# Optimization experiments

Measured on AMD Instinct MI355X. Metric: run time of the kernel, lower is better.

The kernel has to match this reference:

```python
import jax, jax.numpy as jnp
import numpy as np

N_NODES = 50000
N_EDGES = 1000000
F = 256          # feature_size
NC = 300         # n_content_dims
ED = 64          # embedding_dim = 2**int(log2(F/4))
L = 3            # n_layers


def setup_inputs() -> dict:
    key = jax.random.key(0)
    ks = jax.random.split(key, 20)
    s = 0.05  # weight init scale
    return {
        'node_ids': jnp.arange(N_NODES, dtype=jnp.int32),
        'content': jax.random.normal(ks[0], (N_NODES, NC), jnp.float32),
        'src': jax.random.randint(ks[1], (N_EDGES,), 0, N_NODES, jnp.int32),
        'dst': jax.random.randint(ks[2], (N_EDGES,), 0, N_NODES, jnp.int32),
        'emb': jax.random.normal(ks[3], (N_NODES + 1, ED), jnp.float32) / ED,
        'W_exp': jax.random.normal(ks[4], (F, ED), jnp.float32) * s,
        'b_exp': jnp.zeros((F,), jnp.float32),
        'W_p1': jax.random.normal(ks[5], (NC, NC), jnp.float32) * s,
        'b_p1': jnp.zeros((NC,), jnp.float32),
        'W_p2': jax.random.normal(ks[6], (F, NC), jnp.float32) * s,
        'b_p2': jnp.zeros((F,), jnp.float32),
        'W_conv': jax.random.normal(ks[7], (L, F, 2 * F), jnp.float32) * s,
        'b_conv': jnp.zeros((L, F), jnp.float32),
        'Wo1': jax.random.normal(ks[8], (L - 1, F, F), jnp.float32) * s,
        'bo1': jnp.zeros((L - 1, F), jnp.float32),
        'Wo2': jax.random.normal(ks[9], (L - 1, F, F), jnp.float32) * s,
        'bo2': jnp.zeros((L - 1, F), jnp.float32),
    }


def _lrelu(x):
    return jax.nn.leaky_relu(x, 0.1)


def reference(node_ids, content, src, dst, emb, W_exp, b_exp, W_p1, b_p1,
              W_p2, b_p2, W_conv, b_conv, Wo1, bo1, Wo2, bo2):
    # initial node repr: expansion(node_emb) + proj(content)  (GaussianNoise = identity at eval)
    h = _lrelu(emb[node_ids] @ W_exp.T + b_exp)                 # [N, F]
    c = _lrelu(content @ W_p1.T + b_p1)
    c = _lrelu(c @ W_p2.T + b_p2)
    h = h + c

    ones = jnp.ones((src.shape[0],), h.dtype)
    deg = jax.ops.segment_sum(ones, dst, num_segments=N_NODES)  # in-degree
    w = (deg + 1.0)[:, None]                                    # +1 for self-loop

    for i in range(L):
        # message passing: sum neighbor h (with self-loop), then neighbor mean
        agg = jax.ops.segment_sum(h[src], dst, num_segments=N_NODES) + h  # [N, F]
        h_agg = (agg - h) / jnp.maximum(w - 1.0, 1.0)
        h_concat = jnp.concatenate([h, h_agg], axis=1)          # [N, 2F]
        h_new = h_concat @ W_conv[i].T + b_conv[i]
        if i < L - 1:
            h_new = _lrelu(h_new)
        # L2-normalize rows
        h_new = h_new / jnp.maximum(
            jnp.linalg.norm(h_new, axis=1, keepdims=True), 1e-6)
        if i < L - 1:  # W_out block (non-prediction layers)
            h_new = _lrelu(h_new @ Wo1[i].T + bo1[i])
            h_new = h_new @ Wo2[i].T + bo2[i]
        h = h_new
    return h
```

## Files before the change

kernel.cpp:

```cpp
#include <hip/hip_runtime.h>
#include <stdint.h>

#define NNODES 50000
#define NROWS_PAD 50048
#define NEDGES 1000000
#define FD 256
#define NCPAD 384
#define EDIM 64
#define NSCAN ((NNODES + 255) / 256)

typedef unsigned short u16;
typedef __attribute__((ext_vector_type(8))) short short8;
typedef __attribute__((ext_vector_type(4))) float floatx4;

__device__ __forceinline__ float bf2f(u16 x) {
    union { unsigned u; float f; } c; c.u = ((unsigned)x) << 16; return c.f;
}
__device__ __forceinline__ u16 f2bf(float f) {
    union { float f; unsigned u; } c; c.f = f;
    unsigned u = c.u;
    return (u16)((u + 0x7fffu + ((u >> 16) & 1u)) >> 16);
}
__device__ __forceinline__ void gload16(const u16* g, u16* l) {
    __builtin_amdgcn_global_load_lds(
        (const __attribute__((address_space(1))) void*)g,
        (__attribute__((address_space(3))) void*)l, 16, 0, 0);
}

__global__ void detect_kernel(const u16* p, int* flag) {
    __shared__ int smax;
    if (threadIdx.x == 0) smax = 0;
    __syncthreads();
    int m = 0;
    for (int i = threadIdx.x; i < 8192; i += 256) {
        int e = (p[i] >> 7) & 0xFF;
        m = m > e ? m : e;
    }
    atomicMax(&smax, m);
    __syncthreads();
    if (threadIdx.x == 0) *flag = (smax >= 140) ? 1 : 0;
}

#define NB_CONV 1798
#define NB_CNT4 489
#define PREP_GRID (NB_CONV + NB_CNT4)
__global__ __launch_bounds__(512) void prep_kernel(
    u16* arena, const int* flagp,
    const void* wexp, const void* bexp, const void* wp1, const void* bp1,
    const void* wp2, const void* bp2, const void* wconv, const void* bconv,
    const void* wo1, const void* bo1, const void* wo2, const void* bo2,
    const int* dst, int* deg)
{
    const int bid = blockIdx.x;
    if (bid >= NB_CONV) {
        int base = ((bid - NB_CONV) * 512 + threadIdx.x) * 4;
        if (base < NEDGES) {
            int4 d = *(const int4*)(dst + base);
            atomicAdd(&deg[d.x], 1);
            atomicAdd(&deg[d.y], 1);
            atomicAdd(&deg[d.z], 1);
            atomicAdd(&deg[d.w], 1);
        }
        return;
    }
    const int offs[13]  = {0,16384,16640,164096,164480,262784,263040,
                           656256,657024,788096,788608,919680,920192};
    const int rreal[12] = {256,1,300,1,256,1,768,1,512,1,512,1};
    const int creal[12] = {64,256,300,300,300,256,512,768,256,512,256,512};
    const int cpd[12]   = {64,256,384,384,384,256,512,768,256,512,256,512};
    long gid = (long)bid * 512 + threadIdx.x;
    if (gid >= 920192) return;
    const void* srcs[12] = {wexp,bexp,wp1,bp1,wp2,bp2,wconv,bconv,wo1,bo1,wo2,bo2};
    int fl = *flagp;
    int t = 0;
    #pragma unroll
    for (int i = 1; i < 12; ++i) if (gid >= offs[i]) t = i;
    long local = gid - offs[t];
    int rr = (int)(local / cpd[t]);
    int cc = (int)(local % cpd[t]);
    u16 v = 0;
    if (rr < rreal[t] && cc < creal[t]) {
        long si = (long)rr * creal[t] + cc;
        v = fl ? f2bf(((const float*)srcs[t])[si]) : ((const u16*)srcs[t])[si];
    }
    arena[gid] = v;
}

__global__ __launch_bounds__(256) void scan1_kernel(const int* deg, int* bsum) {
    __shared__ int s[256];
    int t = threadIdx.x;
    int i = blockIdx.x * 256 + t;
    s[t] = (i < NNODES) ? deg[i] : 0;
    __syncthreads();
    #pragma unroll
    for (int off = 128; off > 0; off >>= 1) {
        if (t < off) s[t] += s[t + off];
        __syncthreads();
    }
    if (t == 0) bsum[blockIdx.x] = s[0];
}

__global__ __launch_bounds__(256) void scan2_kernel(int* bsum, int* row_start) {
    __shared__ int s[256];
    int t = threadIdx.x;
    int v = (t < NSCAN) ? bsum[t] : 0;
    s[t] = v;
    __syncthreads();
    for (int off = 1; off < 256; off <<= 1) {
        int x = (t >= off) ? s[t - off] : 0;
        __syncthreads();
        s[t] += x;
        __syncthreads();
    }
    if (t < NSCAN) bsum[t] = s[t] - v;
    if (t == 0) row_start[NNODES] = NEDGES;
}

__global__ __launch_bounds__(256) void scan3_kernel(const int* deg, const int* bsum,
        int* row_start, int* cursor, float* inv_w) {
    __shared__ int s[256];
    int t = threadIdx.x;
    int i = blockIdx.x * 256 + t;
    int v = (i < NNODES) ? deg[i] : 0;
    s[t] = v;
    __syncthreads();
    for (int off = 1; off < 256; off <<= 1) {
        int x = (t >= off) ? s[t - off] : 0;
        __syncthreads();
        s[t] += x;
        __syncthreads();
    }
    if (i < NNODES) {
        int base = bsum[blockIdx.x] + s[t] - v;
        row_start[i] = base;
        cursor[i] = base;
        inv_w[i] = 1.0f / (float)(v > 0 ? v : 1);
    }
}

#define IF_GRID (391 * 7)
__global__ __launch_bounds__(512, 4) void initfill_kernel(
    const void* __restrict__ content, const void* __restrict__ emb,
    const int* __restrict__ flagp,
    const u16* __restrict__ Wp1, const u16* __restrict__ bp1,
    const u16* __restrict__ Wp2, const u16* __restrict__ bp2,
    const u16* __restrict__ Wexp, const u16* __restrict__ bexp,
    u16* __restrict__ hbuf,
    const int* __restrict__ src, const int* __restrict__ dst,
    int* __restrict__ cursor, int* __restrict__ esrc)
{
    __shared__ __align__(16) u16 sA[64 * 64];
    __shared__ __align__(16) u16 sB[384 * 32];
    __shared__ __align__(16) u16 T[64 * 384];

    const int g7 = blockIdx.x / 7, r7 = blockIdx.x % 7;
    if (r7 >= 2) {
        int fb = g7 * 5 + (r7 - 2);
        int e = fb * 512 + threadIdx.x;
        if (e < NEDGES) {
            int v = dst[e];
            int pos = atomicAdd(&cursor[v], 1);
            if ((unsigned)pos < (unsigned)NEDGES) esrc[pos] = src[e];
        }
        return;
    }
    const int bm = (g7 * 2 + r7) * 64;
    const int t = threadIdx.x;
    const int wave = t >> 6, lane = t & 63;
    const int quad = lane >> 4, l16 = lane & 15;
    const int wm = wave >> 2, wn = wave & 3;
    const int lrow = lane >> 2, lcol = (lane & 3) * 8;
    const int fl = *flagp;

    {
        int row = t >> 3;
        int c0 = (t & 7) * 8;
        int gm = bm + row;
        u16 o[8];
        if (gm < NNODES) {
            if (fl) {
                const float* ep = (const float*)emb + (size_t)gm * EDIM + c0;
                float4 x = *(const float4*)ep;
                float4 y = *(const float4*)(ep + 4);
                o[0]=f2bf(x.x); o[1]=f2bf(x.y); o[2]=f2bf(x.z); o[3]=f2bf(x.w);
                o[4]=f2bf(y.x); o[5]=f2bf(y.y); o[6]=f2bf(y.z); o[7]=f2bf(y.w);
            } else {
                const u16* ep = (const u16*)emb + (size_t)gm * EDIM + c0;
                ushort4 x = *(const ushort4*)ep;
                ushort4 y = *(const ushort4*)(ep + 4);
                o[0]=x.x; o[1]=x.y; o[2]=x.z; o[3]=x.w;
                o[4]=y.x; o[5]=y.y; o[6]=y.z; o[7]=y.w;
            }
        } else {
            #pragma unroll
            for (int k = 0; k < 8; ++k) o[k] = 0;
        }
        u16* d = &sA[(row * 64 + c0) ^ ((row & 7) << 3)];
        *(ushort4*)d = (ushort4){o[0], o[1], o[2], o[3]};
        *(ushort4*)(d + 4) = (ushort4){o[4], o[5], o[6], o[7]};
    }
    #pragma unroll
    for (int j = 0; j < 6; ++j) {
        int idx = (j * 512 + t) * 8;
        int row = idx / 384;
        int c0 = idx % 384;
        int gm = bm + row;
        u16 o[8];
        if (gm < NNODES && c0 + 8 <= 300) {
            if (fl) {
                const float* cp = (const float*)content + (size_t)gm * 300 + c0;
                float4 x = *(const float4*)cp;
                float4 y = *(const float4*)(cp + 4);
                o[0]=f2bf(x.x); o[1]=f2bf(x.y); o[2]=f2bf(x.z); o[3]=f2bf(x.w);
                o[4]=f2bf(y.x); o[5]=f2bf(y.y); o[6]=f2bf(y.z); o[7]=f2bf(y.w);
            } else {
                const u16* cp = (const u16*)content + (size_t)gm * 300 + c0;
                ushort4 x = *(const ushort4*)cp;
                ushort4 y = *(const ushort4*)(cp + 4);
                o[0]=x.x; o[1]=x.y; o[2]=x.z; o[3]=x.w;
                o[4]=y.x; o[5]=y.y; o[6]=y.z; o[7]=y.w;
            }
        } else if (gm < NNODES && c0 < 300) {
            #pragma unroll
            for (int k = 0; k < 8; ++k) {
                int c = c0 + k;
                o[k] = (c < 300)
                    ? (fl ? f2bf(((const float*)content)[(size_t)gm * 300 + c])
                          : ((const u16*)content)[(size_t)gm * 300 + c])
                    : (u16)0;
            }
        } else {
            #pragma unroll
            for (int k = 0; k < 8; ++k) o[k] = 0;
        }
        u16* d = &T[(row * 384 + c0) ^ ((row & 7) << 3)];
        *(ushort4*)d = (ushort4){o[0], o[1], o[2], o[3]};
        *(ushort4*)(d + 4) = (ushort4){o[4], o[5], o[6], o[7]};
    }
    __syncthreads();

    floatx4 a1[2][6];
    #pragma unroll
    for (int i = 0; i < 2; ++i)
        #pragma unroll
        for (int j = 0; j < 6; ++j) a1[i][j] = (floatx4){0.f, 0.f, 0.f, 0.f};
    for (int kt = 0; kt < 384; kt += 32) {
        #pragma unroll
        for (int c = 0; c < 3; ++c) {
            int r0 = wave * 48 + c * 16;
            gload16(Wp1 + (size_t)(r0 + lrow) * NCPAD + kt + lcol, &sB[r0 * 32]);
        }
        __syncthreads();
        short8 af[2];
        #pragma unroll
        for (int mt = 0; mt < 2; ++mt) {
            int row = wm * 32 + mt * 16 + l16;
            af[mt] = *(const short8*)&T[(row * 384 + kt + quad * 8) ^ ((row & 7) << 3)];
        }
        #pragma unroll
        for (int nt = 0; nt < 6; ++nt) {
            short8 bf = *(const short8*)&sB[(wn * 96 + nt * 16 + l16) * 32 + quad * 8];
            a1[0][nt] = __builtin_amdgcn_mfma_f32_16x16x32_bf16(af[0], bf, a1[0][nt], 0, 0, 0);
            a1[1][nt] = __builtin_amdgcn_mfma_f32_16x16x32_bf16(af[1], bf, a1[1][nt], 0, 0, 0);
        }
        __syncthreads();
    }
    #pragma unroll
    for (int nt = 0; nt < 6; ++nt) {
        int col = wn * 96 + nt * 16 + l16;
        float bv = bf2f(bp1[col]);
        #pragma unroll
        for (int mt = 0; mt < 2; ++mt)
            #pragma unroll
            for (int rr = 0; rr < 4; ++rr) {
                int row = wm * 32 + mt * 16 + quad * 4 + rr;
                float v = a1[mt][nt][rr] + bv;
                v = v > 0.f ? v : 0.1f * v;
                T[(row * NCPAD + col) ^ ((row & 7) << 3)] = f2bf(v);
            }
    }
    __syncthreads();

    floatx4 a2[2][4];
    #pragma unroll
    for (int i = 0; i < 2; ++i)
        #pragma unroll
        for (int j = 0; j < 4; ++j) a2[i][j] = (floatx4){0.f, 0.f, 0.f, 0.f};
    for (int kt = 0; kt < 384; kt += 32) {
        #pragma unroll
        for (int c = 0; c < 2; ++c) {
            int r0 = wave * 32 + c * 16;
            gload16(Wp2 + (size_t)(r0 + lrow) * NCPAD + kt + lcol, &sB[r0 * 32]);
        }
        __syncthreads();
        short8 af[2];
        #pragma unroll
        for (int mt = 0; mt < 2; ++mt) {
            int row = wm * 32 + mt * 16 + l16;
            af[mt] = *(const short8*)&T[(row * NCPAD + kt + quad * 8) ^ ((row & 7) << 3)];
        }
        #pragma unroll
        for (int nt = 0; nt < 4; ++nt) {
            short8 bf = *(const short8*)&sB[(wn * 64 + nt * 16 + l16) * 32 + quad * 8];
            a2[0][nt] = __builtin_amdgcn_mfma_f32_16x16x32_bf16(af[0], bf, a2[0][nt], 0, 0, 0);
            a2[1][nt] = __builtin_amdgcn_mfma_f32_16x16x32_bf16(af[1], bf, a2[1][nt], 0, 0, 0);
        }
        __syncthreads();
    }

    floatx4 aE[2][4];
    #pragma unroll
    for (int i = 0; i < 2; ++i)
        #pragma unroll
        for (int j = 0; j < 4; ++j) aE[i][j] = (floatx4){0.f, 0.f, 0.f, 0.f};
    for (int kt = 0; kt < 64; kt += 32) {
        #pragma unroll
        for (int c = 0; c < 2; ++c) {
            int r0 = wave * 32 + c * 16;
            gload16(Wexp + (size_t)(r0 + lrow) * EDIM + kt + lcol, &sB[r0 * 32]);
        }
        __syncthreads();
        short8 af[2];
        #pragma unroll
        for (int mt = 0; mt < 2; ++mt) {
            int row = wm * 32 + mt * 16 + l16;
            af[mt] = *(const short8*)&sA[(row * 64 + kt + quad * 8) ^ ((row & 7) << 3)];
        }
        #pragma unroll
        for (int nt = 0; nt < 4; ++nt) {
            short8 bf = *(const short8*)&sB[(wn * 64 + nt * 16 + l16) * 32 + quad * 8];
            aE[0][nt] = __builtin_amdgcn_mfma_f32_16x16x32_bf16(af[0], bf, aE[0][nt], 0, 0, 0);
            aE[1][nt] = __builtin_amdgcn_mfma_f32_16x16x32_bf16(af[1], bf, aE[1][nt], 0, 0, 0);
        }
        __syncthreads();
    }

    #pragma unroll
    for (int nt = 0; nt < 4; ++nt) {
        int col = wn * 64 + nt * 16 + l16;
        float bE = bf2f(bexp[col]), b2 = bf2f(bp2[col]);
        #pragma unroll
        for (int mt = 0; mt < 2; ++mt)
            #pragma unroll
            for (int rr = 0; rr < 4; ++rr) {
                int row = wm * 32 + mt * 16 + quad * 4 + rr;
                int gm = bm + row;
                if (gm < NNODES) {
                    float hE = aE[mt][nt][rr] + bE; hE = hE > 0.f ? hE : 0.1f * hE;
                    float c2 = a2[mt][nt][rr] + b2; c2 = c2 > 0.f ? c2 : 0.1f * c2;
                    hbuf[(size_t)gm * FD + col] = f2bf(hE + c2);
                }
            }
    }
}

__global__ __launch_bounds__(512, 4) void layer_kernel(
    const u16* __restrict__ h, const u16* __restrict__ agg,
    const u16* __restrict__ Wc, const u16* __restrict__ bc,
    const u16* __restrict__ W1, const u16* __restrict__ b1,
    const u16* __restrict__ W2, const u16* __restrict__ b2,
    u16* __restrict__ out)
{
    __shared__ __align__(16) u16 sA[2][64 * 32];
    __shared__ __align__(16) u16 sB[2][256 * 32];
    __shared__ __align__(16) u16 T[64 * 256];
    __shared__ float ssq[4][64];

    const int t = threadIdx.x;
    const int wave = t >> 6, lane = t & 63;
    const int quad = lane >> 4, l16 = lane & 15;
    const int wm = wave >> 2, wn = wave & 3;
    const int lrow = lane >> 2, lcol = (lane & 3) * 8;
    const int bm = blockIdx.x * 64;

    floatx4 acc[2][4];
    #pragma unroll
    for (int i = 0; i < 2; ++i)
        #pragma unroll
        for (int j = 0; j < 4; ++j) acc[i][j] = (floatx4){0.f, 0.f, 0.f, 0.f};

    for (int kt = 0; kt < 512; kt += 64) {
        const u16* Ap = (kt < 256) ? h : agg;
        const int kk = kt & 255;
        {
            int hh = wave & 1, r0 = (wave >> 1) * 16;
            gload16(Ap + (size_t)(bm + r0 + lrow) * 256 + kk + hh * 32 + lcol,
                    &sA[hh][r0 * 32]);
        }
        #pragma unroll
        for (int c = 0; c < 4; ++c) {
            int hh = c >> 1, r0 = wave * 32 + (c & 1) * 16;
            gload16(Wc + (size_t)(r0 + lrow) * 512 + kt + hh * 32 + lcol,
                    &sB[hh][r0 * 32]);
        }
        __syncthreads();
        #pragma unroll
        for (int g = 0; g < 2; ++g) {
            short8 af[2], bf[4];
            #pragma unroll
            for (int mt = 0; mt < 2; ++mt)
                af[mt] = *(const short8*)&sA[g][(wm * 32 + mt * 16 + l16) * 32 + quad * 8];
            #pragma unroll
            for (int nt = 0; nt < 4; ++nt)
                bf[nt] = *(const short8*)&sB[g][(wn * 64 + nt * 16 + l16) * 32 + quad * 8];
            #pragma unroll
            for (int mt = 0; mt < 2; ++mt)
                #pragma unroll
                for (int nt = 0; nt < 4; ++nt)
                    acc[mt][nt] = __builtin_amdgcn_mfma_f32_16x16x32_bf16(af[mt], bf[nt], acc[mt][nt], 0, 0, 0);
        }
        __syncthreads();
    }
    {
        float part[2][4];
        #pragma unroll
        for (int mt = 0; mt < 2; ++mt)
            #pragma unroll
            for (int rr = 0; rr < 4; ++rr) part[mt][rr] = 0.f;
        #pragma unroll
        for (int nt = 0; nt < 4; ++nt) {
            float bv = bf2f(bc[wn * 64 + nt * 16 + l16]);
            #pragma unroll
            for (int mt = 0; mt < 2; ++mt)
                #pragma unroll
                for (int rr = 0; rr < 4; ++rr) {
                    float v = acc[mt][nt][rr] + bv;
                    v = v > 0.f ? v : 0.1f * v;
                    part[mt][rr] += v * v;
                }
        }
        #pragma unroll
        for (int off = 1; off < 16; off <<= 1)
            #pragma unroll
            for (int mt = 0; mt < 2; ++mt)
                #pragma unroll
                for (int rr = 0; rr < 4; ++rr)
                    part[mt][rr] += __shfl_xor(part[mt][rr], off);
        if (l16 == 0)
            #pragma unroll
            for (int mt = 0; mt < 2; ++mt)
                #pragma unroll
                for (int rr = 0; rr < 4; ++rr)
                    ssq[wn][wm * 32 + mt * 16 + quad * 4 + rr] = part[mt][rr];
        __syncthreads();
        #pragma unroll
        for (int mt = 0; mt < 2; ++mt)
            #pragma unroll
            for (int rr = 0; rr < 4; ++rr) {
                int row = wm * 32 + mt * 16 + quad * 4 + rr;
                float s = 1.0f / fmaxf(sqrtf(ssq[0][row] + ssq[1][row] +
                                             ssq[2][row] + ssq[3][row]), 1e-6f);
                #pragma unroll
                for (int nt = 0; nt < 4; ++nt) {
                    int col = wn * 64 + nt * 16 + l16;
                    float v = acc[mt][nt][rr] + bf2f(bc[col]);
                    v = v > 0.f ? v : 0.1f * v;
                    T[(row * 256 + col) ^ ((row & 7) << 3)] = f2bf(v * s);
                }
            }
        __syncthreads();
    }

    #pragma unroll
    for (int i = 0; i < 2; ++i)
        #pragma unroll
        for (int j = 0; j < 4; ++j) acc[i][j] = (floatx4){0.f, 0.f, 0.f, 0.f};
    for (int kt = 0; kt < 256; kt += 64) {
        #pragma unroll
        for (int c = 0; c < 4; ++c) {
            int hh = c >> 1, r0 = wave * 32 + (c & 1) * 16;
            gload16(W1 + (size_t)(r0 + lrow) * 256 + kt + hh * 32 + lcol,
                    &sB[hh][r0 * 32]);
        }
        __syncthreads();
        #pragma unroll
        for (int g = 0; g < 2; ++g) {
            short8 af[2], bf[4];
            #pragma unroll
            for (int mt = 0; mt < 2; ++mt) {
                int row = wm * 32 + mt * 16 + l16;
                af[mt] = *(const short8*)&T[(row * 256 + kt + g * 32 + quad * 8) ^ ((row & 7) << 3)];
            }
            #pragma unroll
            for (int nt = 0; nt < 4; ++nt)
                bf[nt] = *(const short8*)&sB[g][(wn * 64 + nt * 16 + l16) * 32 + quad * 8];
            #pragma unroll
            for (int mt = 0; mt < 2; ++mt)
                #pragma unroll
                for (int nt = 0; nt < 4; ++nt)
                    acc[mt][nt] = __builtin_amdgcn_mfma_f32_16x16x32_bf16(af[mt], bf[nt], acc[mt][nt], 0, 0, 0);
        }
        __syncthreads();
    }
    #pragma unroll
    for (int nt = 0; nt < 4; ++nt) {
        int col = wn * 64 + nt * 16 + l16;
        float bv = bf2f(b1[col]);
        #pragma unroll
        for (int mt = 0; mt < 2; ++mt) {
            #pragma unroll
            for (int r = 0; r < 4; ++r) {
                int row = wm * 32 + mt * 16 + quad * 4 + r;
                float v = acc[mt][nt][r] + bv;
                v = v > 0.f ? v : 0.1f * v;
                T[(row * 256 + col) ^ ((row & 7) << 3)] = f2bf(v);
            }
        }
    }
    __syncthreads();

    #pragma unroll
    for (int i = 0; i < 2; ++i)
        #pragma unroll
        for (int j = 0; j < 4; ++j) acc[i][j] = (floatx4){0.f, 0.f, 0.f, 0.f};
    for (int kt = 0; kt < 256; kt += 64) {
        #pragma unroll
        for (int c = 0; c < 4; ++c) {
            int hh = c >> 1, r0 = wave * 32 + (c & 1) * 16;
            gload16(W2 + (size_t)(r0 + lrow) * 256 + kt + hh * 32 + lcol,
                    &sB[hh][r0 * 32]);
        }
        __syncthreads();
        #pragma unroll
        for (int g = 0; g < 2; ++g) {
            short8 af[2], bf[4];
            #pragma unroll
            for (int mt = 0; mt < 2; ++mt) {
                int row = wm * 32 + mt * 16 + l16;
                af[mt] = *(const short8*)&T[(row * 256 + kt + g * 32 + quad * 8) ^ ((row & 7) << 3)];
            }
            #pragma unroll
            for (int nt = 0; nt < 4; ++nt)
                bf[nt] = *(const short8*)&sB[g][(wn * 64 + nt * 16 + l16) * 32 + quad * 8];
            #pragma unroll
            for (int mt = 0; mt < 2; ++mt)
                #pragma unroll
                for (int nt = 0; nt < 4; ++nt)
                    acc[mt][nt] = __builtin_amdgcn_mfma_f32_16x16x32_bf16(af[mt], bf[nt], acc[mt][nt], 0, 0, 0);
        }
        __syncthreads();
    }
    #pragma unroll
    for (int nt = 0; nt < 4; ++nt) {
        int col = wn * 64 + nt * 16 + l16;
        float bv = bf2f(b2[col]);
        #pragma unroll
        for (int mt = 0; mt < 2; ++mt) {
            #pragma unroll
            for (int r = 0; r < 4; ++r) {
                int row = wm * 32 + mt * 16 + quad * 4 + r;
                int gm = bm + row;
                if (gm < NNODES) {
                    float v = acc[mt][nt][r] + bv;
                    out[(size_t)gm * 256 + col] = f2bf(v);
                }
            }
        }
    }
}

__global__ __launch_bounds__(512, 4) void final_kernel(
    const u16* __restrict__ h, const u16* __restrict__ agg,
    const u16* __restrict__ Wc, const u16* __restrict__ bc,
    float* __restrict__ out)
{
    __shared__ __align__(16) u16 sA[2][64 * 32];
    __shared__ __align__(16) u16 sB[2][256 * 32];
    __shared__ float ssq[4][64];

    const int t = threadIdx.x;
    const int wave = t >> 6, lane = t & 63;
    const int quad = lane >> 4, l16 = lane & 15;
    const int wm = wave >> 2, wn = wave & 3;
    const int lrow = lane >> 2, lcol = (lane & 3) * 8;
    const int bm = blockIdx.x * 64;

    floatx4 acc[2][4];
    #pragma unroll
    for (int i = 0; i < 2; ++i)
        #pragma unroll
        for (int j = 0; j < 4; ++j) acc[i][j] = (floatx4){0.f, 0.f, 0.f, 0.f};

    for (int kt = 0; kt < 512; kt += 64) {
        const u16* Ap = (kt < 256) ? h : agg;
        const int kk = kt & 255;
        {
            int hh = wave & 1, r0 = (wave >> 1) * 16;
            gload16(Ap + (size_t)(bm + r0 + lrow) * 256 + kk + hh * 32 + lcol,
                    &sA[hh][r0 * 32]);
        }
        #pragma unroll
        for (int c = 0; c < 4; ++c) {
            int hh = c >> 1, r0 = wave * 32 + (c & 1) * 16;
            gload16(Wc + (size_t)(r0 + lrow) * 512 + kt + hh * 32 + lcol,
                    &sB[hh][r0 * 32]);
        }
        __syncthreads();
        #pragma unroll
        for (int g = 0; g < 2; ++g) {
            short8 af[2], bf[4];
            #pragma unroll
            for (int mt = 0; mt < 2; ++mt)
                af[mt] = *(const short8*)&sA[g][(wm * 32 + mt * 16 + l16) * 32 + quad * 8];
            #pragma unroll
            for (int nt = 0; nt < 4; ++nt)
                bf[nt] = *(const short8*)&sB[g][(wn * 64 + nt * 16 + l16) * 32 + quad * 8];
            #pragma unroll
            for (int mt = 0; mt < 2; ++mt)
                #pragma unroll
                for (int nt = 0; nt < 4; ++nt)
                    acc[mt][nt] = __builtin_amdgcn_mfma_f32_16x16x32_bf16(af[mt], bf[nt], acc[mt][nt], 0, 0, 0);
        }
        __syncthreads();
    }
    float part[2][4];
    #pragma unroll
    for (int mt = 0; mt < 2; ++mt)
        #pragma unroll
        for (int rr = 0; rr < 4; ++rr) part[mt][rr] = 0.f;
    #pragma unroll
    for (int nt = 0; nt < 4; ++nt) {
        float bv = bf2f(bc[wn * 64 + nt * 16 + l16]);
        #pragma unroll
        for (int mt = 0; mt < 2; ++mt)
            #pragma unroll
            for (int rr = 0; rr < 4; ++rr) {
                float v = acc[mt][nt][rr] + bv;
                part[mt][rr] += v * v;
            }
    }
    #pragma unroll
    for (int off = 1; off < 16; off <<= 1)
        #pragma unroll
        for (int mt = 0; mt < 2; ++mt)
            #pragma unroll
            for (int rr = 0; rr < 4; ++rr)
                part[mt][rr] += __shfl_xor(part[mt][rr], off);
    if (l16 == 0)
        #pragma unroll
        for (int mt = 0; mt < 2; ++mt)
            #pragma unroll
            for (int rr = 0; rr < 4; ++rr)
                ssq[wn][wm * 32 + mt * 16 + quad * 4 + rr] = part[mt][rr];
    __syncthreads();
    #pragma unroll
    for (int mt = 0; mt < 2; ++mt)
        #pragma unroll
        for (int rr = 0; rr < 4; ++rr) {
            int row = wm * 32 + mt * 16 + quad * 4 + rr;
            int gm = bm + row;
            float s = 1.0f / fmaxf(sqrtf(ssq[0][row] + ssq[1][row] +
                                         ssq[2][row] + ssq[3][row]), 1e-6f);
            if (gm < NNODES) {
                #pragma unroll
                for (int nt = 0; nt < 4; ++nt) {
                    int col = wn * 64 + nt * 16 + l16;
                    out[(size_t)gm * 256 + col] = (acc[mt][nt][rr] + bf2f(bc[col])) * s;
                }
            }
        }
}

__global__ __launch_bounds__(256) void agg_kernel(
    const u16* h, const int* row_start, const int* esrc,
    const float* inv_w, u16* out)
{
    int gid = blockIdx.x * blockDim.x + threadIdx.x;
    int wid = __builtin_amdgcn_readfirstlane(gid >> 6);
    int lane = threadIdx.x & 63;
    if (wid >= NNODES) return;
    int e0 = row_start[wid], e1 = row_start[wid + 1];
    e0 = max(0, min(e0, NEDGES));
    e1 = max(e0, min(e1, NEDGES));
    float a0 = 0.f, a1 = 0.f, a2 = 0.f, a3 = 0.f;
    int e = e0;
    for (; e + 8 <= e1; e += 8) {
        int u[8];
        #pragma unroll
        for (int k = 0; k < 8; ++k) {
            u[k] = esrc[e + k];
            if ((unsigned)u[k] >= (unsigned)NNODES) u[k] = 0;
        }
        ushort4 tv[8];
        #pragma unroll
        for (int k = 0; k < 8; ++k)
            tv[k] = *(const ushort4*)(h + (size_t)u[k] * FD + lane * 4);
        #pragma unroll
        for (int k = 0; k < 8; ++k) {
            a0 += bf2f(tv[k].x); a1 += bf2f(tv[k].y);
            a2 += bf2f(tv[k].z); a3 += bf2f(tv[k].w);
        }
    }
    for (; e + 2 <= e1; e += 2) {
        int u0 = esrc[e + 0]; if ((unsigned)u0 >= (unsigned)NNODES) u0 = 0;
        int u1 = esrc[e + 1]; if ((unsigned)u1 >= (unsigned)NNODES) u1 = 0;
        ushort4 t0 = *(const ushort4*)(h + (size_t)u0 * FD + lane * 4);
        ushort4 t1 = *(const ushort4*)(h + (size_t)u1 * FD + lane * 4);
        a0 += bf2f(t0.x) + bf2f(t1.x);
        a1 += bf2f(t0.y) + bf2f(t1.y);
        a2 += bf2f(t0.z) + bf2f(t1.z);
        a3 += bf2f(t0.w) + bf2f(t1.w);
    }
    for (; e < e1; ++e) {
        int u = esrc[e];
        if ((unsigned)u >= (unsigned)NNODES) u = 0;
        ushort4 tv = *(const ushort4*)(h + (size_t)u * FD + lane * 4);
        a0 += bf2f(tv.x); a1 += bf2f(tv.y); a2 += bf2f(tv.z); a3 += bf2f(tv.w);
    }
    float s = inv_w[wid];
    ushort4 ov;
    ov.x = f2bf(a0 * s); ov.y = f2bf(a1 * s); ov.z = f2bf(a2 * s); ov.w = f2bf(a3 * s);
    *(ushort4*)(out + (size_t)wid * FD + lane * 4) = ov;
}

extern "C" void kernel_launch(void* const* d_in, const int* in_sizes, int n_in,
                              void* d_out, int out_size, void* d_ws, size_t ws_size,
                              hipStream_t stream) {
    const void* content = d_in[1];
    const int* src      = (const int*)d_in[2];
    const int* dst      = (const int*)d_in[3];
    const void* emb     = d_in[4];

    char* ws = (char*)d_ws;
    u16* arena = (u16*)(ws);
    u16* hbuf  = (u16*)(ws + 1840640);
    u16* buf2  = (u16*)(ws + 27465216);
    int*   deg    = (int*)(ws + 78714368);
    int*   rs     = (int*)(ws + 78914560);
    int*   cursor = (int*)(ws + 79114752);
    float* inv_w  = (float*)(ws + 79314944);
    int*   esrc   = (int*)(ws + 79515136);
    int*   bsum   = (int*)(ws + 83515648);
    int*   flag   = (int*)(ws + 83516672);

    u16* aWexp  = arena;            u16* aBexp  = arena + 16384;
    u16* aWp1   = arena + 16640;    u16* aBp1   = arena + 164096;
    u16* aWp2   = arena + 164480;   u16* aBp2   = arena + 262784;
    u16* aWconv = arena + 263040;   u16* aBconv = arena + 656256;
    u16* aWo1   = arena + 657024;   u16* aBo1   = arena + 788096;
    u16* aWo2   = arena + 788608;   u16* aBo2   = arena + 919680;

    const int MB64 = NROWS_PAD / 64;

    detect_kernel<<<1, 256, 0, stream>>>((const u16*)content, flag);
    hipMemsetAsync(deg, 0, (size_t)NNODES * 4, stream);
    prep_kernel<<<PREP_GRID, 512, 0, stream>>>(arena, flag,
        d_in[5], d_in[6], d_in[7], d_in[8], d_in[9], d_in[10], d_in[11],
        d_in[12], d_in[13], d_in[14], d_in[15], d_in[16], dst, deg);

    scan1_kernel<<<NSCAN, 256, 0, stream>>>(deg, bsum);
    scan2_kernel<<<1, 256, 0, stream>>>(bsum, rs);
    scan3_kernel<<<NSCAN, 256, 0, stream>>>(deg, bsum, rs, cursor, inv_w);

    initfill_kernel<<<IF_GRID, 512, 0, stream>>>(content, emb, flag,
        aWp1, aBp1, aWp2, aBp2, aWexp, aBexp, hbuf, src, dst, cursor, esrc);

    for (int i = 0; i < 3; ++i) {
        agg_kernel<<<(NNODES * 64) / 256, 256, 0, stream>>>(hbuf, rs, esrc, inv_w, buf2);
        if (i < 2) {
            layer_kernel<<<dim3(MB64), dim3(512), 0, stream>>>(
                hbuf, buf2,
                aWconv + (size_t)i * FD * 2 * FD, aBconv + (size_t)i * FD,
                aWo1 + (size_t)i * FD * FD, aBo1 + (size_t)i * FD,
                aWo2 + (size_t)i * FD * FD, aBo2 + (size_t)i * FD,
                hbuf);
        } else {
            final_kernel<<<dim3(MB64), dim3(512), 0, stream>>>(
                hbuf, buf2,
                aWconv + (size_t)i * FD * 2 * FD, aBconv + (size_t)i * FD,
                (float*)d_out);
        }
    }
}
```

Measured before the change: 651.3 us.

## Shrink GEMM K-tile to raise occupancy and fuse prologue launches

The layer and final GEMM kernels now stage a single 32-wide K slice instead of two, which halves the shared-memory tiles and raises the launch-bounds occupancy hint from 4 to 6 blocks. The degree memset is folded into the detect kernel, and the two scan kernels after the block-sum pass are merged so each block reduces its own prefix of block sums. These cuts are meant to remove launch overhead and let more blocks overlap memory latency. In exchange there are twice as many barriers per K loop and less work between each sync.

```diff
diff --git a/kernel.cpp b/kernel.cpp
--- a/kernel.cpp
+++ b/kernel.cpp
@@ -27,13 +27,16 @@
         (__attribute__((address_space(3))) void*)l, 16, 0, 0);
 }
 
-__global__ void detect_kernel(const u16* p, int* flag) {
+__global__ __launch_bounds__(256) void detect_kernel(const u16* p, int* flag, int* deg) {
+    int i = blockIdx.x * 256 + threadIdx.x;
+    if (i < NNODES) deg[i] = 0;
+    if (blockIdx.x != 0) return;
     __shared__ int smax;
     if (threadIdx.x == 0) smax = 0;
     __syncthreads();
     int m = 0;
-    for (int i = threadIdx.x; i < 8192; i += 256) {
-        int e = (p[i] >> 7) & 0xFF;
+    for (int k = threadIdx.x; k < 8192; k += 256) {
+        int e = (p[k] >> 7) & 0xFF;
         m = m > e ? m : e;
     }
     atomicMax(&smax, m);
@@ -100,11 +103,25 @@
     if (t == 0) bsum[blockIdx.x] = s[0];
 }
 
-__global__ __launch_bounds__(256) void scan2_kernel(int* bsum, int* row_start) {
+__global__ __launch_bounds__(256) void scan23_kernel(const int* deg, const int* bsum,
+        int* row_start, int* cursor, float* inv_w) {
     __shared__ int s[256];
+    __shared__ int sbase;
     int t = threadIdx.x;
-    int v = (t < NSCAN) ? bsum[t] : 0;
+    int b = blockIdx.x;
+    int v = (t < b && t < NSCAN) ? bsum[t] : 0;
     s[t] = v;
+    __syncthreads();
+    #pragma unroll
+    for (int off = 128; off > 0; off >>= 1) {
+        if (t < off) s[t] += s[t + off];
+        __syncthreads();
+    }
+    if (t == 0) sbase = s[0];
+    __syncthreads();
+    int i = b * 256 + t;
+    int d = (i < NNODES) ? deg[i] : 0;
+    s[t] = d;
     __syncthreads();
     for (int off = 1; off < 256; off <<= 1) {
         int x = (t >= off) ? s[t - off] : 0;
@@ -112,30 +129,13 @@
         s[t] += x;
         __syncthreads();
     }
-    if (t < NSCAN) bsum[t] = s[t] - v;
-    if (t == 0) row_start[NNODES] = NEDGES;
-}
-
-__global__ __launch_bounds__(256) void scan3_kernel(const int* deg, const int* bsum,
-        int* row_start, int* cursor, float* inv_w) {
-    __shared__ int s[256];
-    int t = threadIdx.x;
-    int i = blockIdx.x * 256 + t;
-    int v = (i < NNODES) ? deg[i] : 0;
-    s[t] = v;
-    __syncthreads();
-    for (int off = 1; off < 256; off <<= 1) {
-        int x = (t >= off) ? s[t - off] : 0;
-        __syncthreads();
-        s[t] += x;
-        __syncthreads();
-    }
     if (i < NNODES) {
-        int base = bsum[blockIdx.x] + s[t] - v;
+        int base = sbase + s[t] - d;
         row_start[i] = base;
         cursor[i] = base;
-        inv_w[i] = 1.0f / (float)(v > 0 ? v : 1);
-    }
+        inv_w[i] = 1.0f / (float)(d > 0 ? d : 1);
+    }
+    if (b == 0 && t == 0) row_start[NNODES] = NEDGES;
 }
 
 #define IF_GRID (391 * 7)
@@ -354,15 +354,15 @@
     }
 }
 
-__global__ __launch_bounds__(512, 4) void layer_kernel(
+__global__ __launch_bounds__(512, 6) void layer_kernel(
     const u16* __restrict__ h, const u16* __restrict__ agg,
     const u16* __restrict__ Wc, const u16* __restrict__ bc,
     const u16* __restrict__ W1, const u16* __restrict__ b1,
     const u16* __restrict__ W2, const u16* __restrict__ b2,
     u16* __restrict__ out)
 {
-    __shared__ __align__(16) u16 sA[2][64 * 32];
-    __shared__ __align__(16) u16 sB[2][256 * 32];
+    __shared__ __align__(16) u16 sA[64 * 32];
+    __shared__ __align__(16) u16 sB[256 * 32];
     __shared__ __align__(16) u16 T[64 * 256];
     __shared__ float ssq[4][64];
 
@@ -379,36 +379,30 @@
         #pragma unroll
         for (int j = 0; j < 4; ++j) acc[i][j] = (floatx4){0.f, 0.f, 0.f, 0.f};
 
-    for (int kt = 0; kt < 512; kt += 64) {
+    for (int kt = 0; kt < 512; kt += 32) {
         const u16* Ap = (kt < 256) ? h : agg;
         const int kk = kt & 255;
-        {
-            int hh = wave & 1, r0 = (wave >> 1) * 16;
-            gload16(Ap + (size_t)(bm + r0 + lrow) * 256 + kk + hh * 32 + lcol,
-                    &sA[hh][r0 * 32]);
-        }
-        #pragma unroll
-        for (int c = 0; c < 4; ++c) {
-            int hh = c >> 1, r0 = wave * 32 + (c & 1) * 16;
-            gload16(Wc + (size_t)(r0 + lrow) * 512 + kt + hh * 32 + lcol,
-                    &sB[hh][r0 * 32]);
-        }
-        __syncthreads();
-        #pragma unroll
-        for (int g = 0; g < 2; ++g) {
-            short8 af[2], bf[4];
-            #pragma unroll
-            for (int mt = 0; mt < 2; ++mt)
-                af[mt] = *(const short8*)&sA[g][(wm * 32 + mt * 16 + l16) * 32 + quad * 8];
+        if (wave < 4)
+            gload16(Ap + (size_t)(bm + wave * 16 + lrow) * 256 + kk + lcol,
+                    &sA[(wave * 16) * 32]);
+        #pragma unroll
+        for (int c = 0; c < 2; ++c) {
+            int r0 = wave * 32 + c * 16;
+            gload16(Wc + (size_t)(r0 + lrow) * 512 + kt + lcol, &sB[r0 * 32]);
+        }
+        __syncthreads();
+        short8 af[2], bf[4];
+        #pragma unroll
+        for (int mt = 0; mt < 2; ++mt)
+            af[mt] = *(const short8*)&sA[(wm * 32 + mt * 16 + l16) * 32 + quad * 8];
+        #pragma unroll
+        for (int nt = 0; nt < 4; ++nt)
+            bf[nt] = *(const short8*)&sB[(wn * 64 + nt * 16 + l16) * 32 + quad * 8];
+        #pragma unroll
+        for (int mt = 0; mt < 2; ++mt)
             #pragma unroll
             for (int nt = 0; nt < 4; ++nt)
-                bf[nt] = *(const short8*)&sB[g][(wn * 64 + nt * 16 + l16) * 32 + quad * 8];
-            #pragma unroll
-            for (int mt = 0; mt < 2; ++mt)
-                #pragma unroll
-                for (int nt = 0; nt < 4; ++nt)
-                    acc[mt][nt] = __builtin_amdgcn_mfma_f32_16x16x32_bf16(af[mt], bf[nt], acc[mt][nt], 0, 0, 0);
-        }
+                acc[mt][nt] = __builtin_amdgcn_mfma_f32_16x16x32_bf16(af[mt], bf[nt], acc[mt][nt], 0, 0, 0);
         __syncthreads();
     }
     {
@@ -465,31 +459,27 @@
     for (int i = 0; i < 2; ++i)
         #pragma unroll
         for (int j = 0; j < 4; ++j) acc[i][j] = (floatx4){0.f, 0.f, 0.f, 0.f};
-    for (int kt = 0; kt < 256; kt += 64) {
-        #pragma unroll
-        for (int c = 0; c < 4; ++c) {
-            int hh = c >> 1, r0 = wave * 32 + (c & 1) * 16;
-            gload16(W1 + (size_t)(r0 + lrow) * 256 + kt + hh * 32 + lcol,
-                    &sB[hh][r0 * 32]);
-        }
-        __syncthreads();
-        #pragma unroll
-        for (int g = 0; g < 2; ++g) {
-            short8 af[2], bf[4];
-            #pragma unroll
-            for (int mt = 0; mt < 2; ++mt) {
-                int row = wm * 32 + mt * 16 + l16;
-                af[mt] = *(const short8*)&T[(row * 256 + kt + g * 32 + quad * 8) ^ ((row & 7) << 3)];
-            }
+    for (int kt = 0; kt < 256; kt += 32) {
+        #pragma unroll
+        for (int c = 0; c < 2; ++c) {
+            int r0 = wave * 32 + c * 16;
+            gload16(W1 + (size_t)(r0 + lrow) * 256 + kt + lcol, &sB[r0 * 32]);
+        }
+        __syncthreads();
+        short8 af[2], bf[4];
+        #pragma unroll
+        for (int mt = 0; mt < 2; ++mt) {
+            int row = wm * 32 + mt * 16 + l16;
+            af[mt] = *(const short8*)&T[(row * 256 + kt + quad * 8) ^ ((row & 7) << 3)];
+        }
+        #pragma unroll
+        for (int nt = 0; nt < 4; ++nt)
+            bf[nt] = *(const short8*)&sB[(wn * 64 + nt * 16 + l16) * 32 + quad * 8];
+        #pragma unroll
+        for (int mt = 0; mt < 2; ++mt)
             #pragma unroll
             for (int nt = 0; nt < 4; ++nt)
-                bf[nt] = *(const short8*)&sB[g][(wn * 64 + nt * 16 + l16) * 32 + quad * 8];
-            #pragma unroll
-            for (int mt = 0; mt < 2; ++mt)
-                #pragma unroll
-                for (int nt = 0; nt < 4; ++nt)
-                    acc[mt][nt] = __builtin_amdgcn_mfma_f32_16x16x32_bf16(af[mt], bf[nt], acc[mt][nt], 0, 0, 0);
-        }
+                acc[mt][nt] = __builtin_amdgcn_mfma_f32_16x16x32_bf16(af[mt], bf[nt], acc[mt][nt], 0, 0, 0);
         __syncthreads();
     }
     #pragma unroll
@@ -513,31 +503,27 @@
     for (int i = 0; i < 2; ++i)
         #pragma unroll
         for (int j = 0; j < 4; ++j) acc[i][j] = (floatx4){0.f, 0.f, 0.f, 0.f};
-    for (int kt = 0; kt < 256; kt += 64) {
-        #pragma unroll
-        for (int c = 0; c < 4; ++c) {
-            int hh = c >> 1, r0 = wave * 32 + (c & 1) * 16;
-            gload16(W2 + (size_t)(r0 + lrow) * 256 + kt + hh * 32 + lcol,
-                    &sB[hh][r0 * 32]);
-        }
-        __syncthreads();
-        #pragma unroll
-        for (int g = 0; g < 2; ++g) {
-            short8 af[2], bf[4];
-            #pragma unroll
-            for (int mt = 0; mt < 2; ++mt) {
-                int row = wm * 32 + mt * 16 + l16;
-                af[mt] = *(const short8*)&T[(row * 256 + kt + g * 32 + quad * 8) ^ ((row & 7) << 3)];
-            }
+    for (int kt = 0; kt < 256; kt += 32) {
+        #pragma unroll
+        for (int c = 0; c < 2; ++c) {
+            int r0 = wave * 32 + c * 16;
+            gload16(W2 + (size_t)(r0 + lrow) * 256 + kt + lcol, &sB[r0 * 32]);
+        }
+        __syncthreads();
+        short8 af[2], bf[4];
+        #pragma unroll
+        for (int mt = 0; mt < 2; ++mt) {
+            int row = wm * 32 + mt * 16 + l16;
+            af[mt] = *(const short8*)&T[(row * 256 + kt + quad * 8) ^ ((row & 7) << 3)];
+        }
+        #pragma unroll
+        for (int nt = 0; nt < 4; ++nt)
+            bf[nt] = *(const short8*)&sB[(wn * 64 + nt * 16 + l16) * 32 + quad * 8];
+        #pragma unroll
+        for (int mt = 0; mt < 2; ++mt)
             #pragma unroll
             for (int nt = 0; nt < 4; ++nt)
-                bf[nt] = *(const short8*)&sB[g][(wn * 64 + nt * 16 + l16) * 32 + quad * 8];
-            #pragma unroll
-            for (int mt = 0; mt < 2; ++mt)
-                #pragma unroll
-                for (int nt = 0; nt < 4; ++nt)
-                    acc[mt][nt] = __builtin_amdgcn_mfma_f32_16x16x32_bf16(af[mt], bf[nt], acc[mt][nt], 0, 0, 0);
-        }
+                acc[mt][nt] = __builtin_amdgcn_mfma_f32_16x16x32_bf16(af[mt], bf[nt], acc[mt][nt], 0, 0, 0);
         __syncthreads();
     }
     #pragma unroll
@@ -559,13 +545,13 @@
     }
 }
 
-__global__ __launch_bounds__(512, 4) void final_kernel(
+__global__ __launch_bounds__(512, 6) void final_kernel(
     const u16* __restrict__ h, const u16* __restrict__ agg,
     const u16* __restrict__ Wc, const u16* __restrict__ bc,
     float* __restrict__ out)
 {
-    __shared__ __align__(16) u16 sA[2][64 * 32];
-    __shared__ __align__(16) u16 sB[2][256 * 32];
+    __shared__ __align__(16) u16 sA[64 * 32];
+    __shared__ __align__(16) u16 sB[256 * 32];
     __shared__ float ssq[4][64];
 
     const int t = threadIdx.x;
@@ -581,36 +567,30 @@
         #pragma unroll
         for (int j = 0; j < 4; ++j) acc[i][j] = (floatx4){0.f, 0.f, 0.f, 0.f};
 
-    for (int kt = 0; kt < 512; kt += 64) {
+    for (int kt = 0; kt < 512; kt += 32) {
         const u16* Ap = (kt < 256) ? h : agg;
         const int kk = kt & 255;
-        {
-            int hh = wave & 1, r0 = (wave >> 1) * 16;
-            gload16(Ap + (size_t)(bm + r0 + lrow) * 256 + kk + hh * 32 + lcol,
-                    &sA[hh][r0 * 32]);
-        }
-        #pragma unroll
-        for (int c = 0; c < 4; ++c) {
-            int hh = c >> 1, r0 = wave * 32 + (c & 1) * 16;
-            gload16(Wc + (size_t)(r0 + lrow) * 512 + kt + hh * 32 + lcol,
-                    &sB[hh][r0 * 32]);
-        }
-        __syncthreads();
-        #pragma unroll
-        for (int g = 0; g < 2; ++g) {
-            short8 af[2], bf[4];
-            #pragma unroll
-            for (int mt = 0; mt < 2; ++mt)
-                af[mt] = *(const short8*)&sA[g][(wm * 32 + mt * 16 + l16) * 32 + quad * 8];
+        if (wave < 4)
+            gload16(Ap + (size_t)(bm + wave * 16 + lrow) * 256 + kk + lcol,
+                    &sA[(wave * 16) * 32]);
+        #pragma unroll
+        for (int c = 0; c < 2; ++c) {
+            int r0 = wave * 32 + c * 16;
+            gload16(Wc + (size_t)(r0 + lrow) * 512 + kt + lcol, &sB[r0 * 32]);
+        }
+        __syncthreads();
+        short8 af[2], bf[4];
+        #pragma unroll
+        for (int mt = 0; mt < 2; ++mt)
+            af[mt] = *(const short8*)&sA[(wm * 32 + mt * 16 + l16) * 32 + quad * 8];
+        #pragma unroll
+        for (int nt = 0; nt < 4; ++nt)
+            bf[nt] = *(const short8*)&sB[(wn * 64 + nt * 16 + l16) * 32 + quad * 8];
+        #pragma unroll
+        for (int mt = 0; mt < 2; ++mt)
             #pragma unroll
             for (int nt = 0; nt < 4; ++nt)
-                bf[nt] = *(const short8*)&sB[g][(wn * 64 + nt * 16 + l16) * 32 + quad * 8];
-            #pragma unroll
-            for (int mt = 0; mt < 2; ++mt)
-                #pragma unroll
-                for (int nt = 0; nt < 4; ++nt)
-                    acc[mt][nt] = __builtin_amdgcn_mfma_f32_16x16x32_bf16(af[mt], bf[nt], acc[mt][nt], 0, 0, 0);
-        }
+                acc[mt][nt] = __builtin_amdgcn_mfma_f32_16x16x32_bf16(af[mt], bf[nt], acc[mt][nt], 0, 0, 0);
         __syncthreads();
     }
     float part[2][4];
@@ -742,15 +722,13 @@
 
     const int MB64 = NROWS_PAD / 64;
 
-    detect_kernel<<<1, 256, 0, stream>>>((const u16*)content, flag);
-    hipMemsetAsync(deg, 0, (size_t)NNODES * 4, stream);
+    detect_kernel<<<NSCAN, 256, 0, stream>>>((const u16*)content, flag, deg);
     prep_kernel<<<PREP_GRID, 512, 0, stream>>>(arena, flag,
         d_in[5], d_in[6], d_in[7], d_in[8], d_in[9], d_in[10], d_in[11],
         d_in[12], d_in[13], d_in[14], d_in[15], d_in[16], dst, deg);
 
     scan1_kernel<<<NSCAN, 256, 0, stream>>>(deg, bsum);
-    scan2_kernel<<<1, 256, 0, stream>>>(bsum, rs);
-    scan3_kernel<<<NSCAN, 256, 0, stream>>>(deg, bsum, rs, cursor, inv_w);
+    scan23_kernel<<<NSCAN, 256, 0, stream>>>(deg, bsum, rs, cursor, inv_w);
 
     initfill_kernel<<<IF_GRID, 512, 0, stream>>>(content, emb, flag,
         aWp1, aBp1, aWp2, aBp2, aWexp, aBexp, hbuf, src, dst, cursor, esrc);
```

Result: slower. 726.8 us (+11.6%).
